# Kernel optimization log

Measured on AMD Instinct MI355X. Metric: run time of the kernel, lower is better.

Reference implementation:

```python
import jax, jax.numpy as jnp
import numpy as np

# hyperparams from __init__
K_SEL = 8          # SoftSelectorProxy K
R_TEMP = 1.0       # SoftSelectorProxy r (temperature)
LAM = 0.5          # SoftSelectorProxy lam (blend)
MAX_PROXY = 16     # max_proxy_points -> K_eff (N >> 16)

B, N, INPUT_DIM = 32, 16384, 64
HID, K_DIM, D_MODEL = 64, 16, 512
ANCHOR_DIM = INPUT_DIM + 2  # structural_feature_dim: x feats + saliency + normalized position


def setup_inputs() -> dict:
    key = jax.random.key(0)
    ks = jax.random.split(key, 10)
    s = lambda k, shp, fan: jax.random.normal(k, shp, jnp.float32) * (1.0 / np.sqrt(fan))
    return {
        "x": jax.random.normal(ks[0], (B, N, INPUT_DIM), jnp.float32),
        "W1": s(ks[1], (INPUT_DIM, HID), INPUT_DIM),
        "b1": jnp.zeros((HID,), jnp.float32),
        "w_e": s(ks[2], (HID,), HID),
        "w_s": s(ks[3], (HID,), HID),
        "W_lift": s(ks[4], (ANCHOR_DIM, K_DIM), ANCHOR_DIM),
        "b_lift": jnp.zeros((K_DIM,), jnp.float32),
        "W_proj": s(ks[5], (K_DIM, D_MODEL), K_DIM),
        "b_proj": jnp.zeros((D_MODEL,), jnp.float32),
        "mu": jnp.zeros((ANCHOR_DIM,), jnp.float32),
        "sigma": jnp.ones((ANCHOR_DIM,), jnp.float32),
    }


def reference(x, W1, b1, w_e, w_s, W_lift, b_lift, W_proj, b_proj, mu, sigma):
    # CausalEventModel: shared hidden, event + saliency heads
    h = jnp.tanh(jnp.einsum('bnd,dh->bnh', x, W1) + b1)          # [B,N,HID]
    saliency = jax.nn.softplus(jnp.einsum('bnh,h->bn', h, w_s))   # [B,N]
    # SoftSelectorProxy: blend of sigmoid gate and K-scaled softmax (soft top-K relaxation)
    y_star = LAM * jax.nn.sigmoid(saliency / R_TEMP) + (1.0 - LAM) * K_SEL * jax.nn.softmax(saliency / R_TEMP, axis=1)  # [B,N]
    # dense_anchor_vectors: concat features, saliency, normalized position
    pos = jnp.broadcast_to((jnp.arange(N, dtype=jnp.float32) / N)[None, :, None], (x.shape[0], N, 1))
    dense = jnp.concatenate([x, saliency[..., None], pos], axis=-1)  # [B,N,ANCHOR_DIM]
    # NormalizedLift: normalize then linear lift to k_dim
    lifted = jnp.einsum('bna,ak->bnk', (dense - mu) / sigma, W_lift) + b_lift  # [B,N,K_DIM]
    # topk selection + gather + projection
    _, top_idx = jax.lax.top_k(y_star, MAX_PROXY)                 # [B,MAX_PROXY]
    cloud = jnp.take_along_axis(lifted, top_idx[..., None], axis=1)  # [B,MAX_PROXY,K_DIM]
    tokens = jnp.einsum('bkc,cd->bkd', cloud, W_proj) + b_proj    # [B,MAX_PROXY,D_MODEL]
    return tokens, y_star
```

## Files before the change

### kernel.cpp

```cpp
#include <hip/hip_runtime.h>
#include <math.h>

#define B 32
#define N 16384
#define DIM 64
#define HID 64
#define KD 16
#define DM 512
#define MP 16

#define GRID_SAL 1024
#define ITERS 8

typedef __attribute__((ext_vector_type(8))) _Float16 f16x8;
typedef __attribute__((ext_vector_type(2))) __fp16 fph2;
typedef __attribute__((ext_vector_type(4))) float f32x4;

__device__ __forceinline__ float fast_tanh(float a) {
  const float e = __expf(2.f * a);
  return 1.f - 2.f * __builtin_amdgcn_rcpf(e + 1.f);
}

__global__ __launch_bounds__(256) void k_saliency(
    const float* __restrict__ x, const float* __restrict__ W1,
    const float* __restrict__ b1, const float* __restrict__ w_s,
    float* __restrict__ sal) {
  const int t = threadIdx.x;
  const int lane = t & 63, wid = t >> 6;
  const int c16 = lane & 15, kq = lane >> 4;

  __shared__ __align__(16) _Float16 lWh[64 * 72];
  __shared__ __align__(16) _Float16 lWl[64 * 72];
  __shared__ __align__(16) float lws[64], lb1[64];
#pragma unroll
  for (int j = 0; j < 16; ++j) {
    const int i = t + 256 * j;
    const int k = i >> 6, col = i & 63;
    const float v = W1[i];
    const _Float16 h = (_Float16)v;
    lWh[col * 72 + k] = h;
    lWl[col * 72 + k] = (_Float16)(v - (float)h);
  }
  if (t < 64) { lws[t] = w_s[t]; lb1[t] = b1[t]; }
  __syncthreads();

  f16x8 WH[8], WL[8];
#pragma unroll
  for (int ct = 0; ct < 4; ++ct)
#pragma unroll
    for (int kc = 0; kc < 2; ++kc) {
      const int off = (ct * 16 + c16) * 72 + kc * 32 + kq * 8;
      WH[ct * 2 + kc] = *(const f16x8*)(lWh + off);
      WL[ct * 2 + kc] = *(const f16x8*)(lWl + off);
    }

#define PKSPLIT(va, vb, HW, LW) {                                                  \
    const fph2 h_ = __builtin_amdgcn_cvt_pkrtz((va), (vb));                        \
    const fph2 l_ = __builtin_amdgcn_cvt_pkrtz((va) - (float)h_[0],                \
                                               (vb) - (float)h_[1]);               \
    HW = __builtin_bit_cast(unsigned, h_);                                         \
    LW = __builtin_bit_cast(unsigned, l_); }

#define SAL_LOADS(b0, b1_, b2, b3, it_) {                                          \
    const size_t row_ = ((size_t)(it_) * GRID_SAL + blockIdx.x) * 64 + wid * 16 + c16; \
    const float* __restrict__ p_ = x + row_ * DIM + kq * 8;                        \
    b0 = *(const float4*)(p_);       b1_ = *(const float4*)(p_ + 4);               \
    b2 = *(const float4*)(p_ + 32);  b3 = *(const float4*)(p_ + 36); }

#define SAL_COMPUTE(b0, b1_, b2, b3, it_) {                                        \
    f32x4 a0 = (f32x4)0.f, a1 = (f32x4)0.f, a2 = (f32x4)0.f, a3 = (f32x4)0.f;      \
    {                                                                  \
      uint4 H, L;                                                                  \
      PKSPLIT(b0.x, b0.y, H.x, L.x); PKSPLIT(b0.z, b0.w, H.y, L.y);                \
      PKSPLIT(b1_.x, b1_.y, H.z, L.z); PKSPLIT(b1_.z, b1_.w, H.w, L.w);            \
      const f16x8 bh = __builtin_bit_cast(f16x8, H);                               \
      const f16x8 bl = __builtin_bit_cast(f16x8, L);                               \
      a0 = __builtin_amdgcn_mfma_f32_16x16x32_f16(WH[0], bh, a0, 0, 0, 0);         \
      a1 = __builtin_amdgcn_mfma_f32_16x16x32_f16(WH[2], bh, a1, 0, 0, 0);         \
      a2 = __builtin_amdgcn_mfma_f32_16x16x32_f16(WH[4], bh, a2, 0, 0, 0);         \
      a3 = __builtin_amdgcn_mfma_f32_16x16x32_f16(WH[6], bh, a3, 0, 0, 0);         \
      a0 = __builtin_amdgcn_mfma_f32_16x16x32_f16(WL[0], bh, a0, 0, 0, 0);         \
      a1 = __builtin_amdgcn_mfma_f32_16x16x32_f16(WL[2], bh, a1, 0, 0, 0);         \
      a2 = __builtin_amdgcn_mfma_f32_16x16x32_f16(WL[4], bh, a2, 0, 0, 0);         \
      a3 = __builtin_amdgcn_mfma_f32_16x16x32_f16(WL[6], bh, a3, 0, 0, 0);         \
      a0 = __builtin_amdgcn_mfma_f32_16x16x32_f16(WH[0], bl, a0, 0, 0, 0);         \
      a1 = __builtin_amdgcn_mfma_f32_16x16x32_f16(WH[2], bl, a1, 0, 0, 0);         \
      a2 = __builtin_amdgcn_mfma_f32_16x16x32_f16(WH[4], bl, a2, 0, 0, 0);         \
      a3 = __builtin_amdgcn_mfma_f32_16x16x32_f16(WH[6], bl, a3, 0, 0, 0);         \
    }                                                                              \
    {                                                                  \
      uint4 H, L;                                                                  \
      PKSPLIT(b2.x, b2.y, H.x, L.x); PKSPLIT(b2.z, b2.w, H.y, L.y);                \
      PKSPLIT(b3.x, b3.y, H.z, L.z); PKSPLIT(b3.z, b3.w, H.w, L.w);                \
      const f16x8 bh = __builtin_bit_cast(f16x8, H);                               \
      const f16x8 bl = __builtin_bit_cast(f16x8, L);                               \
      a0 = __builtin_amdgcn_mfma_f32_16x16x32_f16(WH[1], bh, a0, 0, 0, 0);         \
      a1 = __builtin_amdgcn_mfma_f32_16x16x32_f16(WH[3], bh, a1, 0, 0, 0);         \
      a2 = __builtin_amdgcn_mfma_f32_16x16x32_f16(WH[5], bh, a2, 0, 0, 0);         \
      a3 = __builtin_amdgcn_mfma_f32_16x16x32_f16(WH[7], bh, a3, 0, 0, 0);         \
      a0 = __builtin_amdgcn_mfma_f32_16x16x32_f16(WL[1], bh, a0, 0, 0, 0);         \
      a1 = __builtin_amdgcn_mfma_f32_16x16x32_f16(WL[3], bh, a1, 0, 0, 0);         \
      a2 = __builtin_amdgcn_mfma_f32_16x16x32_f16(WL[5], bh, a2, 0, 0, 0);         \
      a3 = __builtin_amdgcn_mfma_f32_16x16x32_f16(WL[7], bh, a3, 0, 0, 0);         \
      a0 = __builtin_amdgcn_mfma_f32_16x16x32_f16(WH[1], bl, a0, 0, 0, 0);         \
      a1 = __builtin_amdgcn_mfma_f32_16x16x32_f16(WH[3], bl, a1, 0, 0, 0);         \
      a2 = __builtin_amdgcn_mfma_f32_16x16x32_f16(WH[5], bl, a2, 0, 0, 0);         \
      a3 = __builtin_amdgcn_mfma_f32_16x16x32_f16(WH[7], bl, a3, 0, 0, 0);         \
    }                                                                              \
    float s = 0.f;                                                                 \
    { const f32x4 wv = *(const f32x4*)(lws + kq * 4);                              \
      const f32x4 bv = *(const f32x4*)(lb1 + kq * 4);                              \
      s = fmaf(wv[0], fast_tanh(a0[0] + bv[0]), s);                                \
      s = fmaf(wv[1], fast_tanh(a0[1] + bv[1]), s);                                \
      s = fmaf(wv[2], fast_tanh(a0[2] + bv[2]), s);                                \
      s = fmaf(wv[3], fast_tanh(a0[3] + bv[3]), s); }                              \
    { const f32x4 wv = *(const f32x4*)(lws + 16 + kq * 4);                         \
      const f32x4 bv = *(const f32x4*)(lb1 + 16 + kq * 4);                         \
      s = fmaf(wv[0], fast_tanh(a1[0] + bv[0]), s);                                \
      s = fmaf(wv[1], fast_tanh(a1[1] + bv[1]), s);                                \
      s = fmaf(wv[2], fast_tanh(a1[2] + bv[2]), s);                                \
      s = fmaf(wv[3], fast_tanh(a1[3] + bv[3]), s); }                              \
    { const f32x4 wv = *(const f32x4*)(lws + 32 + kq * 4);                         \
      const f32x4 bv = *(const f32x4*)(lb1 + 32 + kq * 4);                         \
      s = fmaf(wv[0], fast_tanh(a2[0] + bv[0]), s);                                \
      s = fmaf(wv[1], fast_tanh(a2[1] + bv[1]), s);                                \
      s = fmaf(wv[2], fast_tanh(a2[2] + bv[2]), s);                                \
      s = fmaf(wv[3], fast_tanh(a2[3] + bv[3]), s); }                              \
    { const f32x4 wv = *(const f32x4*)(lws + 48 + kq * 4);                         \
      const f32x4 bv = *(const f32x4*)(lb1 + 48 + kq * 4);                         \
      s = fmaf(wv[0], fast_tanh(a3[0] + bv[0]), s);                                \
      s = fmaf(wv[1], fast_tanh(a3[1] + bv[1]), s);                                \
      s = fmaf(wv[2], fast_tanh(a3[2] + bv[2]), s);                                \
      s = fmaf(wv[3], fast_tanh(a3[3] + bv[3]), s); }                              \
    s += __shfl_xor(s, 16);                                                        \
    s += __shfl_xor(s, 32);                                                        \
    if (lane < 16) {                                                               \
      const size_t sr_ = ((size_t)(it_) * GRID_SAL + blockIdx.x) * 64 + wid * 16 + lane; \
      const float z_ = __expf(-fabsf(s));                                          \
      sal[sr_] = fmaxf(s, 0.f) + __logf(1.f + z_);                                 \
    } }

  float4 pA0, pA1, pA2, pA3;
  float4 pB0, pB1, pB2, pB3;

  SAL_LOADS(pA0, pA1, pA2, pA3, 0);
#pragma unroll 1
  for (int it2 = 0; it2 < ITERS; it2 += 2) {
    SAL_LOADS(pB0, pB1, pB2, pB3, it2 + 1);
    SAL_COMPUTE(pA0, pA1, pA2, pA3, it2);
    if (it2 + 2 < ITERS) SAL_LOADS(pA0, pA1, pA2, pA3, it2 + 2);
    SAL_COMPUTE(pB0, pB1, pB2, pB3, it2 + 1);
  }
#undef SAL_LOADS
#undef SAL_COMPUTE
#undef PKSPLIT
}

__global__ __launch_bounds__(1024) void k_rowfinal(
    float* __restrict__ y,
    const float* __restrict__ x,
    const float* __restrict__ W_lift, const float* __restrict__ b_lift,
    const float* __restrict__ W_proj, const float* __restrict__ b_proj,
    const float* __restrict__ mu, const float* __restrict__ sigma,
    float* __restrict__ tokens) {
  __shared__ float sb[16], ss[16];
  __shared__ float cv[16][16];
  __shared__ int   ci[16][16];
  __shared__ float s_val[MP];
  __shared__ int   s_idx[MP];
  __shared__ float lifted[MP][KD + 1];
  const int b = blockIdx.x, t = threadIdx.x;
  const int wvid = t >> 6, lane = t & 63;
  float* __restrict__ row = y + (size_t)b * N;

  float v[16];
#pragma unroll
  for (int j = 0; j < 16; ++j) v[j] = row[t + 1024 * j];

  float m = v[0];
#pragma unroll
  for (int j = 1; j < 16; ++j) m = fmaxf(m, v[j]);
#pragma unroll
  for (int off = 1; off < 64; off <<= 1) m = fmaxf(m, __shfl_xor(m, off));
  if (lane == 0) sb[wvid] = m;
  __syncthreads();
  m = sb[0];
#pragma unroll
  for (int w = 1; w < 16; ++w) m = fmaxf(m, sb[w]);

  float se = 0.f;
#pragma unroll
  for (int j = 0; j < 16; ++j) se += __expf(v[j] - m);
#pragma unroll
  for (int off = 1; off < 64; off <<= 1) se += __shfl_xor(se, off);
  if (lane == 0) ss[wvid] = se;
  __syncthreads();
  float S = ss[0];
#pragma unroll
  for (int w = 1; w < 16; ++w) S += ss[w];
  const float inv = __builtin_amdgcn_rcpf(S);

#pragma unroll
  for (int j = 0; j < 16; ++j) {
    const float sv = v[j];
    const float sig = __builtin_amdgcn_rcpf(1.f + __expf(-sv));
    row[t + 1024 * j] = fmaf(0.5f, sig, 4.f * __expf(sv - m) * inv);
  }

  for (int k = 0; k < MP; ++k) {
    float bv = v[0]; int bj = 0;
#pragma unroll
    for (int j = 1; j < 16; ++j)
      if (v[j] > bv) { bv = v[j]; bj = j; }
    int bi = t + 1024 * bj;
#pragma unroll
    for (int off = 1; off < 64; off <<= 1) {
      const float ov = __shfl_xor(bv, off);
      const int   oi = __shfl_xor(bi, off);
      if (ov > bv || (ov == bv && oi < bi)) { bv = ov; bi = oi; }
    }
    if (lane == 0) { cv[wvid][k] = bv; ci[wvid][k] = bi; }
#pragma unroll
    for (int jj = 0; jj < 16; ++jj)
      if (bi == t + 1024 * jj) v[jj] = -INFINITY;
  }
  __syncthreads();

  if (wvid == 0) {
    float mv[4]; int mi[4];
#pragma unroll
    for (int q = 0; q < 4; ++q) {
      const int c = lane + 64 * q;
      mv[q] = cv[c >> 4][c & 15];
      mi[q] = ci[c >> 4][c & 15];
    }
    for (int k = 0; k < MP; ++k) {
      float bv = mv[0]; int bi = mi[0];
#pragma unroll
      for (int q = 1; q < 4; ++q)
        if (mv[q] > bv || (mv[q] == bv && mi[q] < bi)) { bv = mv[q]; bi = mi[q]; }
#pragma unroll
      for (int off = 1; off < 64; off <<= 1) {
        const float ov = __shfl_xor(bv, off);
        const int   oi = __shfl_xor(bi, off);
        if (ov > bv || (ov == bv && oi < bi)) { bv = ov; bi = oi; }
      }
      if (lane == 0) { s_val[k] = bv; s_idx[k] = bi; }
#pragma unroll
      for (int q = 0; q < 4; ++q)
        if (mi[q] == bi) mv[q] = -INFINITY;
    }
  }
  __syncthreads();

  if (t < 256) {
    const int p = t >> 4, kd = t & 15;
    const int idx = s_idx[p];
    const float salv = s_val[p];
    const float* __restrict__ xr = x + ((size_t)b * N + idx) * DIM;
    float a = b_lift[kd];
#pragma unroll 8
    for (int d = 0; d < DIM; ++d)
      a = fmaf((xr[d] - mu[d]) * __builtin_amdgcn_rcpf(sigma[d]), W_lift[d * KD + kd], a);
    a = fmaf((salv - mu[64]) * __builtin_amdgcn_rcpf(sigma[64]), W_lift[64 * KD + kd], a);
    a = fmaf(((float)idx * (1.f / (float)N) - mu[65]) * __builtin_amdgcn_rcpf(sigma[65]),
             W_lift[65 * KD + kd], a);
    lifted[p][kd] = a;
  }
  __syncthreads();

  const int d2 = t & 255, pg = t >> 8;
  const float2* __restrict__ Wp2 = (const float2*)W_proj;
  const float2 bp = ((const float2*)b_proj)[d2];
#pragma unroll
  for (int q = 0; q < 4; ++q) {
    const int p2 = pg * 4 + q;
    float2 o = bp;
#pragma unroll
    for (int c = 0; c < KD; ++c) {
      const float2 w = Wp2[c * 256 + d2];
      o.x = fmaf(lifted[p2][c], w.x, o.x);
      o.y = fmaf(lifted[p2][c], w.y, o.y);
    }
    ((float2*)(tokens + ((size_t)b * MP + p2) * DM))[d2] = o;
  }
}

extern "C" void kernel_launch(void* const* d_in, const int* in_sizes, int n_in,
                              void* d_out, int out_size, void* d_ws, size_t ws_size,
                              hipStream_t stream) {
  const float* x      = (const float*)d_in[0];
  const float* W1     = (const float*)d_in[1];
  const float* b1     = (const float*)d_in[2];
  const float* w_s    = (const float*)d_in[4];
  const float* W_lift = (const float*)d_in[5];
  const float* b_lift = (const float*)d_in[6];
  const float* W_proj = (const float*)d_in[7];
  const float* b_proj = (const float*)d_in[8];
  const float* mu     = (const float*)d_in[9];
  const float* sigma  = (const float*)d_in[10];

  float* tokens = (float*)d_out;
  float* ystar  = (float*)d_out + (size_t)B * MP * DM;

  k_saliency<<<GRID_SAL, 256, 0, stream>>>(x, W1, b1, w_s, ystar);
  k_rowfinal<<<B, 1024, 0, stream>>>(ystar, x, W_lift, b_lift,
                                     W_proj, b_proj, mu, sigma, tokens);
}
```

Measured before the change: 73.06 us.

## Fuse saliency and row finalization into one kernel with last-block-done reduction

Merges the saliency kernel and the per-row softmax/top-k kernel into a single launch. Each block now covers a contiguous 512-point chunk of one batch row. It computes a partial max, a partial exp-sum and a local top-16 in registers, then writes them to a workspace. An atomic counter per row lets the last finishing block combine the partials, normalize y_star, merge the candidates, and do the lift and projection. This removes the second launch and the full reread of the saliency row for max/sum/top-k. In exchange it adds a memset, atomics and fences, and the final per-row work is serialized in a 256-thread block.

Result: slower. 232.4 us (+218.1%).

```diff
diff --git a/kernel.cpp b/kernel.cpp
--- a/kernel.cpp
+++ b/kernel.cpp
@@ -10,7 +10,6 @@
 #define MP 16
 
 #define GRID_SAL 1024
-#define ITERS 8
 
 typedef __attribute__((ext_vector_type(8))) _Float16 f16x8;
 typedef __attribute__((ext_vector_type(2))) __fp16 fph2;
@@ -21,17 +20,31 @@
   return 1.f - 2.f * __builtin_amdgcn_rcpf(e + 1.f);
 }
 
-__global__ __launch_bounds__(256) void k_saliency(
+__global__ __launch_bounds__(256) void k_all(
     const float* __restrict__ x, const float* __restrict__ W1,
     const float* __restrict__ b1, const float* __restrict__ w_s,
-    float* __restrict__ sal) {
+    float* __restrict__ y, float* __restrict__ tokens,
+    const float* __restrict__ W_lift, const float* __restrict__ b_lift,
+    const float* __restrict__ W_proj, const float* __restrict__ b_proj,
+    const float* __restrict__ mu, const float* __restrict__ sigma,
+    int* __restrict__ flags, float* __restrict__ pmax, float* __restrict__ psum,
+    float* __restrict__ cval, int* __restrict__ cidx) {
   const int t = threadIdx.x;
-  const int lane = t & 63, wid = t >> 6;
+  const int lane = t & 63, wvid = t >> 6;
   const int c16 = lane & 15, kq = lane >> 4;
+  const int blk = blockIdx.x;
+  const size_t pbase = (size_t)blk * 512;
 
   __shared__ __align__(16) _Float16 lWh[64 * 72];
   __shared__ __align__(16) _Float16 lWl[64 * 72];
   __shared__ __align__(16) float lws[64], lb1[64];
+  __shared__ float cv[4][16];  __shared__ int ci[4][16];
+  __shared__ float sbm[4], sbs[4];
+  __shared__ int s_old;
+  __shared__ float fm[32], fs[32], fwv[4], s_val[MP];
+  __shared__ int fwi[4], s_idx[MP];
+  __shared__ float lifted[MP][KD + 1];
+
 #pragma unroll
   for (int j = 0; j < 16; ++j) {
     const int i = t + 256 * j;
@@ -61,16 +74,15 @@
     HW = __builtin_bit_cast(unsigned, h_);                                         \
     LW = __builtin_bit_cast(unsigned, l_); }
 
-#define SAL_LOADS(b0, b1_, b2, b3, it_) {                                          \
-    const size_t row_ = ((size_t)(it_) * GRID_SAL + blockIdx.x) * 64 + wid * 16 + c16; \
+#define LDX(b0, b1_, b2, b3, it_) {                                                \
+    const size_t row_ = pbase + (it_) * 64 + wvid * 16 + c16;                      \
     const float* __restrict__ p_ = x + row_ * DIM + kq * 8;                        \
     b0 = *(const float4*)(p_);       b1_ = *(const float4*)(p_ + 4);               \
     b2 = *(const float4*)(p_ + 32);  b3 = *(const float4*)(p_ + 36); }
 
-#define SAL_COMPUTE(b0, b1_, b2, b3, it_) {                                        \
+#define CMP(b0, b1_, b2, b3, it_, OUT) {                                           \
     f32x4 a0 = (f32x4)0.f, a1 = (f32x4)0.f, a2 = (f32x4)0.f, a3 = (f32x4)0.f;      \
-    {                                                                  \
-      uint4 H, L;                                                                  \
+    { uint4 H, L;                                                                  \
       PKSPLIT(b0.x, b0.y, H.x, L.x); PKSPLIT(b0.z, b0.w, H.y, L.y);                \
       PKSPLIT(b1_.x, b1_.y, H.z, L.z); PKSPLIT(b1_.z, b1_.w, H.w, L.w);            \
       const f16x8 bh = __builtin_bit_cast(f16x8, H);                               \
@@ -86,10 +98,8 @@
       a0 = __builtin_amdgcn_mfma_f32_16x16x32_f16(WH[0], bl, a0, 0, 0, 0);         \
       a1 = __builtin_amdgcn_mfma_f32_16x16x32_f16(WH[2], bl, a1, 0, 0, 0);         \
       a2 = __builtin_amdgcn_mfma_f32_16x16x32_f16(WH[4], bl, a2, 0, 0, 0);         \
-      a3 = __builtin_amdgcn_mfma_f32_16x16x32_f16(WH[6], bl, a3, 0, 0, 0);         \
-    }                                                                              \
-    {                                                                  \
-      uint4 H, L;                                                                  \
+      a3 = __builtin_amdgcn_mfma_f32_16x16x32_f16(WH[6], bl, a3, 0, 0, 0); }       \
+    { uint4 H, L;                                                                  \
       PKSPLIT(b2.x, b2.y, H.x, L.x); PKSPLIT(b2.z, b2.w, H.y, L.y);                \
       PKSPLIT(b3.x, b3.y, H.z, L.z); PKSPLIT(b3.z, b3.w, H.w, L.w);                \
       const f16x8 bh = __builtin_bit_cast(f16x8, H);                               \
@@ -105,8 +115,7 @@
       a0 = __builtin_amdgcn_mfma_f32_16x16x32_f16(WH[1], bl, a0, 0, 0, 0);         \
       a1 = __builtin_amdgcn_mfma_f32_16x16x32_f16(WH[3], bl, a1, 0, 0, 0);         \
       a2 = __builtin_amdgcn_mfma_f32_16x16x32_f16(WH[5], bl, a2, 0, 0, 0);         \
-      a3 = __builtin_amdgcn_mfma_f32_16x16x32_f16(WH[7], bl, a3, 0, 0, 0);         \
-    }                                                                              \
+      a3 = __builtin_amdgcn_mfma_f32_16x16x32_f16(WH[7], bl, a3, 0, 0, 0); }       \
     float s = 0.f;                                                                 \
     { const f32x4 wv = *(const f32x4*)(lws + kq * 4);                              \
       const f32x4 bv = *(const f32x4*)(lb1 + kq * 4);                              \
@@ -134,85 +143,59 @@
       s = fmaf(wv[3], fast_tanh(a3[3] + bv[3]), s); }                              \
     s += __shfl_xor(s, 16);                                                        \
     s += __shfl_xor(s, 32);                                                        \
+    OUT = s;                                                                       \
     if (lane < 16) {                                                               \
-      const size_t sr_ = ((size_t)(it_) * GRID_SAL + blockIdx.x) * 64 + wid * 16 + lane; \
       const float z_ = __expf(-fabsf(s));                                          \
-      sal[sr_] = fmaxf(s, 0.f) + __logf(1.f + z_);                                 \
+      y[pbase + (it_) * 64 + wvid * 16 + lane] =                                   \
+          fmaxf(s, 0.f) + __logf(1.f + z_);                          \
     } }
 
-  float4 pA0, pA1, pA2, pA3;
-  float4 pB0, pB1, pB2, pB3;
-
-  SAL_LOADS(pA0, pA1, pA2, pA3, 0);
-#pragma unroll 1
-  for (int it2 = 0; it2 < ITERS; it2 += 2) {
-    SAL_LOADS(pB0, pB1, pB2, pB3, it2 + 1);
-    SAL_COMPUTE(pA0, pA1, pA2, pA3, it2);
-    if (it2 + 2 < ITERS) SAL_LOADS(pA0, pA1, pA2, pA3, it2 + 2);
-    SAL_COMPUTE(pB0, pB1, pB2, pB3, it2 + 1);
-  }
-#undef SAL_LOADS
-#undef SAL_COMPUTE
+  float4 A0, A1, A2, A3, P0, P1, P2, P3;
+  float v0, v1, v2, v3, v4, v5, v6, v7;
+
+  LDX(A0, A1, A2, A3, 0)
+  LDX(P0, P1, P2, P3, 1) CMP(A0, A1, A2, A3, 0, v0)
+  LDX(A0, A1, A2, A3, 2) CMP(P0, P1, P2, P3, 1, v1)
+  LDX(P0, P1, P2, P3, 3) CMP(A0, A1, A2, A3, 2, v2)
+  LDX(A0, A1, A2, A3, 4) CMP(P0, P1, P2, P3, 3, v3)
+  LDX(P0, P1, P2, P3, 5) CMP(A0, A1, A2, A3, 4, v4)
+  LDX(A0, A1, A2, A3, 6) CMP(P0, P1, P2, P3, 5, v5)
+  LDX(P0, P1, P2, P3, 7) CMP(A0, A1, A2, A3, 6, v6)
+  CMP(P0, P1, P2, P3, 7, v7)
+#undef LDX
+#undef CMP
 #undef PKSPLIT
-}
-
-__global__ __launch_bounds__(1024) void k_rowfinal(
-    float* __restrict__ y,
-    const float* __restrict__ x,
-    const float* __restrict__ W_lift, const float* __restrict__ b_lift,
-    const float* __restrict__ W_proj, const float* __restrict__ b_proj,
-    const float* __restrict__ mu, const float* __restrict__ sigma,
-    float* __restrict__ tokens) {
-  __shared__ float sb[16], ss[16];
-  __shared__ float cv[16][16];
-  __shared__ int   ci[16][16];
-  __shared__ float s_val[MP];
-  __shared__ int   s_idx[MP];
-  __shared__ float lifted[MP][KD + 1];
-  const int b = blockIdx.x, t = threadIdx.x;
-  const int wvid = t >> 6, lane = t & 63;
-  float* __restrict__ row = y + (size_t)b * N;
-
-  float v[16];
-#pragma unroll
-  for (int j = 0; j < 16; ++j) v[j] = row[t + 1024 * j];
-
-  float m = v[0];
-#pragma unroll
-  for (int j = 1; j < 16; ++j) m = fmaxf(m, v[j]);
-#pragma unroll
-  for (int off = 1; off < 64; off <<= 1) m = fmaxf(m, __shfl_xor(m, off));
-  if (lane == 0) sb[wvid] = m;
-  __syncthreads();
-  m = sb[0];
-#pragma unroll
-  for (int w = 1; w < 16; ++w) m = fmaxf(m, sb[w]);
-
-  float se = 0.f;
-#pragma unroll
-  for (int j = 0; j < 16; ++j) se += __expf(v[j] - m);
-#pragma unroll
-  for (int off = 1; off < 64; off <<= 1) se += __shfl_xor(se, off);
-  if (lane == 0) ss[wvid] = se;
-  __syncthreads();
-  float S = ss[0];
-#pragma unroll
-  for (int w = 1; w < 16; ++w) S += ss[w];
-  const float inv = __builtin_amdgcn_rcpf(S);
-
-#pragma unroll
-  for (int j = 0; j < 16; ++j) {
-    const float sv = v[j];
-    const float sig = __builtin_amdgcn_rcpf(1.f + __expf(-sv));
-    row[t + 1024 * j] = fmaf(0.5f, sig, 4.f * __expf(sv - m) * inv);
-  }
+
+  const bool holder = (lane < 16);
+
+  float tmax = -INFINITY;
+  if (holder)
+    tmax = fmaxf(fmaxf(fmaxf(v0, v1), fmaxf(v2, v3)),
+                 fmaxf(fmaxf(v4, v5), fmaxf(v6, v7)));
+#pragma unroll
+  for (int off = 1; off < 64; off <<= 1) tmax = fmaxf(tmax, __shfl_xor(tmax, off));
+  if (lane == 0) sbm[wvid] = tmax;
+  __syncthreads();
+  const float bm = fmaxf(fmaxf(sbm[0], sbm[1]), fmaxf(sbm[2], sbm[3]));
+  float tsum = 0.f;
+  if (holder)
+    tsum = __expf(v0 - bm) + __expf(v1 - bm) + __expf(v2 - bm) + __expf(v3 - bm) +
+           __expf(v4 - bm) + __expf(v5 - bm) + __expf(v6 - bm) + __expf(v7 - bm);
+#pragma unroll
+  for (int off = 1; off < 64; off <<= 1) tsum += __shfl_xor(tsum, off);
+  if (lane == 0) sbs[wvid] = tsum;
 
   for (int k = 0; k < MP; ++k) {
-    float bv = v[0]; int bj = 0;
-#pragma unroll
-    for (int j = 1; j < 16; ++j)
-      if (v[j] > bv) { bv = v[j]; bj = j; }
-    int bi = t + 1024 * bj;
+    float bv = v0; int bt = 0;
+    if (v1 > bv) { bv = v1; bt = 1; }
+    if (v2 > bv) { bv = v2; bt = 2; }
+    if (v3 > bv) { bv = v3; bt = 3; }
+    if (v4 > bv) { bv = v4; bt = 4; }
+    if (v5 > bv) { bv = v5; bt = 5; }
+    if (v6 > bv) { bv = v6; bt = 6; }
+    if (v7 > bv) { bv = v7; bt = 7; }
+    int bi = holder ? (int)pbase + bt * 64 + wvid * 16 + lane : 0x7fffffff;
+    if (!holder) bv = -INFINITY;
 #pragma unroll
     for (int off = 1; off < 64; off <<= 1) {
       const float ov = __shfl_xor(bv, off);
@@ -220,69 +203,122 @@
       if (ov > bv || (ov == bv && oi < bi)) { bv = ov; bi = oi; }
     }
     if (lane == 0) { cv[wvid][k] = bv; ci[wvid][k] = bi; }
-#pragma unroll
-    for (int jj = 0; jj < 16; ++jj)
-      if (bi == t + 1024 * jj) v[jj] = -INFINITY;
-  }
-  __syncthreads();
+    if (holder) {
+      const int rel = bi - (int)pbase - wvid * 16 - lane;
+      if (rel == 0) v0 = -INFINITY;
+      else if (rel == 64) v1 = -INFINITY;
+      else if (rel == 128) v2 = -INFINITY;
+      else if (rel == 192) v3 = -INFINITY;
+      else if (rel == 256) v4 = -INFINITY;
+      else if (rel == 320) v5 = -INFINITY;
+      else if (rel == 384) v6 = -INFINITY;
+      else if (rel == 448) v7 = -INFINITY;
+    }
+  }
+  __syncthreads();
+  const float bs = sbs[0] + sbs[1] + sbs[2] + sbs[3];
 
   if (wvid == 0) {
-    float mv[4]; int mi[4];
-#pragma unroll
-    for (int q = 0; q < 4; ++q) {
-      const int c = lane + 64 * q;
-      mv[q] = cv[c >> 4][c & 15];
-      mi[q] = ci[c >> 4][c & 15];
-    }
+    float mv = cv[lane >> 4][lane & 15];
+    int   mi2 = ci[lane >> 4][lane & 15];
     for (int k = 0; k < MP; ++k) {
-      float bv = mv[0]; int bi = mi[0];
-#pragma unroll
-      for (int q = 1; q < 4; ++q)
-        if (mv[q] > bv || (mv[q] == bv && mi[q] < bi)) { bv = mv[q]; bi = mi[q]; }
+      float bv = mv; int bi = mi2;
 #pragma unroll
       for (int off = 1; off < 64; off <<= 1) {
         const float ov = __shfl_xor(bv, off);
         const int   oi = __shfl_xor(bi, off);
         if (ov > bv || (ov == bv && oi < bi)) { bv = ov; bi = oi; }
       }
-      if (lane == 0) { s_val[k] = bv; s_idx[k] = bi; }
-#pragma unroll
-      for (int q = 0; q < 4; ++q)
-        if (mi[q] == bi) mv[q] = -INFINITY;
-    }
-  }
-  __syncthreads();
-
-  if (t < 256) {
+      if (lane == 0) { cval[blk * 16 + k] = bv; cidx[blk * 16 + k] = bi; }
+      if (mi2 == bi) mv = -INFINITY;
+    }
+    if (lane == 0) { pmax[blk] = bm; psum[blk] = bs; }
+  }
+  __syncthreads();
+  __threadfence();
+
+  if (t == 0)
+    s_old = __hip_atomic_fetch_add(&flags[blk >> 5], 1,
+                                   __ATOMIC_ACQ_REL, __HIP_MEMORY_SCOPE_AGENT);
+  __syncthreads();
+  if (s_old != 31) return;
+
+  __threadfence();
+  const int brow = blk >> 5;
+
+  if (t < 32) { fm[t] = pmax[brow * 32 + t]; fs[t] = psum[brow * 32 + t]; }
+  __syncthreads();
+  float m = fm[0];
+#pragma unroll
+  for (int w = 1; w < 32; ++w) m = fmaxf(m, fm[w]);
+  float S = 0.f;
+#pragma unroll
+  for (int c = 0; c < 32; ++c) S += fs[c] * __expf(fm[c] - m);
+  const float inv = __builtin_amdgcn_rcpf(S);
+
+  float4* __restrict__ rowp = (float4*)(y + (size_t)brow * N);
+#pragma unroll
+  for (int j = 0; j < 16; ++j) {
+    float4 f = rowp[t + 256 * j];
+    f.x = fmaf(0.5f, __builtin_amdgcn_rcpf(1.f + __expf(-f.x)), 4.f * __expf(f.x - m) * inv);
+    f.y = fmaf(0.5f, __builtin_amdgcn_rcpf(1.f + __expf(-f.y)), 4.f * __expf(f.y - m) * inv);
+    f.z = fmaf(0.5f, __builtin_amdgcn_rcpf(1.f + __expf(-f.z)), 4.f * __expf(f.z - m) * inv);
+    f.w = fmaf(0.5f, __builtin_amdgcn_rcpf(1.f + __expf(-f.w)), 4.f * __expf(f.w - m) * inv);
+    rowp[t + 256 * j] = f;
+  }
+
+  float mv0 = cval[brow * 512 + t];       int mi0 = cidx[brow * 512 + t];
+  float mv1 = cval[brow * 512 + 256 + t]; int mi1 = cidx[brow * 512 + 256 + t];
+  for (int k = 0; k < MP; ++k) {
+    float bv = mv0; int bi = mi0;
+    if (mv1 > bv || (mv1 == bv && mi1 < bi)) { bv = mv1; bi = mi1; }
+#pragma unroll
+    for (int off = 1; off < 64; off <<= 1) {
+      const float ov = __shfl_xor(bv, off);
+      const int   oi = __shfl_xor(bi, off);
+      if (ov > bv || (ov == bv && oi < bi)) { bv = ov; bi = oi; }
+    }
+    if (lane == 0) { fwv[wvid] = bv; fwi[wvid] = bi; }
+    __syncthreads();
+    float Bv = fwv[0]; int Bi = fwi[0];
+#pragma unroll
+    for (int w = 1; w < 4; ++w)
+      if (fwv[w] > Bv || (fwv[w] == Bv && fwi[w] < Bi)) { Bv = fwv[w]; Bi = fwi[w]; }
+    if (t == 0) { s_val[k] = Bv; s_idx[k] = Bi; }
+    if (mi0 == Bi) mv0 = -INFINITY;
+    if (mi1 == Bi) mv1 = -INFINITY;
+    __syncthreads();
+  }
+
+  {
     const int p = t >> 4, kd = t & 15;
-    const int idx = s_idx[p];
+    const int gidx = s_idx[p];
+    const int n = gidx & (N - 1);
     const float salv = s_val[p];
-    const float* __restrict__ xr = x + ((size_t)b * N + idx) * DIM;
+    const float* __restrict__ xr = x + ((size_t)brow * N + n) * DIM;
     float a = b_lift[kd];
 #pragma unroll 8
     for (int d = 0; d < DIM; ++d)
       a = fmaf((xr[d] - mu[d]) * __builtin_amdgcn_rcpf(sigma[d]), W_lift[d * KD + kd], a);
     a = fmaf((salv - mu[64]) * __builtin_amdgcn_rcpf(sigma[64]), W_lift[64 * KD + kd], a);
-    a = fmaf(((float)idx * (1.f / (float)N) - mu[65]) * __builtin_amdgcn_rcpf(sigma[65]),
+    a = fmaf(((float)n * (1.f / (float)N) - mu[65]) * __builtin_amdgcn_rcpf(sigma[65]),
              W_lift[65 * KD + kd], a);
     lifted[p][kd] = a;
   }
   __syncthreads();
 
-  const int d2 = t & 255, pg = t >> 8;
   const float2* __restrict__ Wp2 = (const float2*)W_proj;
-  const float2 bp = ((const float2*)b_proj)[d2];
-#pragma unroll
-  for (int q = 0; q < 4; ++q) {
-    const int p2 = pg * 4 + q;
+  const float2 bp = ((const float2*)b_proj)[t];
+#pragma unroll 1
+  for (int p2 = 0; p2 < MP; ++p2) {
     float2 o = bp;
 #pragma unroll
     for (int c = 0; c < KD; ++c) {
-      const float2 w = Wp2[c * 256 + d2];
+      const float2 w = Wp2[c * 256 + t];
       o.x = fmaf(lifted[p2][c], w.x, o.x);
       o.y = fmaf(lifted[p2][c], w.y, o.y);
     }
-    ((float2*)(tokens + ((size_t)b * MP + p2) * DM))[d2] = o;
+    ((float2*)(tokens + ((size_t)brow * MP + p2) * DM))[t] = o;
   }
 }
 
@@ -303,7 +339,14 @@
   float* tokens = (float*)d_out;
   float* ystar  = (float*)d_out + (size_t)B * MP * DM;
 
-  k_saliency<<<GRID_SAL, 256, 0, stream>>>(x, W1, b1, w_s, ystar);
-  k_rowfinal<<<B, 1024, 0, stream>>>(ystar, x, W_lift, b_lift,
-                                     W_proj, b_proj, mu, sigma, tokens);
+  int*   flags = (int*)d_ws;
+  float* pmax  = (float*)d_ws + 32;
+  float* psum  = pmax + 1024;
+  float* cval  = psum + 1024;
+  int*   cidx  = (int*)(cval + 16384);
+
+  (void)hipMemsetAsync(flags, 0, 32 * sizeof(int), stream);
+  k_all<<<GRID_SAL, 256, 0, stream>>>(x, W1, b1, w_s, ystar, tokens,
+                                      W_lift, b_lift, W_proj, b_proj, mu, sigma,
+                                      flags, pmax, psum, cval, cidx);
 }
```
